# Kernel tuning notes

Hardware: AMD Instinct MI355X
Metric: run time of the kernel (lower is better)

## Reference

```python
import jax, jax.numpy as jnp
import numpy as np

D_MODEL = 1024
BASE = 7
NUM_PLANES = 2
EPS = 1e-6


def setup_inputs() -> dict:
    key = jax.random.key(0)
    k_x, k_w, k_t, k_g = jax.random.split(key, 4)
    B, S, D = 4, 8192, D_MODEL
    x = jax.random.normal(k_x, (B, S, D), dtype=jnp.float32)
    # eidosTransform params: linear 3D -> D, then 2 planes of learned rotation angles over D/2 pairs
    W = jax.random.normal(k_w, (3 * D, D), dtype=jnp.float32) / np.sqrt(3 * D)
    b = jnp.zeros((D,), dtype=jnp.float32)
    theta = jax.random.normal(k_t, (NUM_PLANES, D // 2), dtype=jnp.float32) * 0.1
    # ModularPhaseNorm gain
    gamma = jnp.ones((D,), dtype=jnp.float32)
    return {"x": x, "W": W, "b": b, "theta": theta, "gamma": gamma}


def _eidos_transform(t, W, b, theta):
    # linear projection 3D -> D ('truncate' collapse to d_out)
    y = jnp.einsum("bse,ed->bsd", t, W) + b  # [B,S,D]
    B, S, D = y.shape
    # geometric mode: rotate (even, odd) dim pairs by learned angles, per plane
    for p in range(NUM_PLANES):
        yp = y.reshape(B, S, D // 2, 2)
        a, c2 = yp[..., 0], yp[..., 1]
        cos_t = jnp.cos(theta[p])
        sin_t = jnp.sin(theta[p])
        ra = a * cos_t - c2 * sin_t
        rb = a * sin_t + c2 * cos_t
        y = jnp.stack([ra, rb], axis=-1).reshape(B, S, D)
    return y


def _modular_phase_norm(y, gamma):
    # RMS-normalize within feature groups defined by (dim index mod BASE)
    D = y.shape[-1]
    group = jnp.arange(D) % BASE                      # [D]
    onehot = jax.nn.one_hot(group, BASE, dtype=y.dtype)  # [D, BASE]
    counts = onehot.sum(axis=0)                       # [BASE]
    ss = jnp.einsum("bsd,dg->bsg", y * y, onehot)     # [B,S,BASE]
    rms = jnp.sqrt(ss / counts + EPS)                 # [B,S,BASE]
    denom = rms[..., group]                           # [B,S,D]
    return y / denom * gamma


def reference(x, W, b, theta, gamma):
    B, S, D = x.shape
    zero_row = jnp.zeros((B, 1, D), dtype=x.dtype)
    left = jnp.concatenate([zero_row, x[:, :-1, :]], axis=1)   # roll +1, zero first
    right = jnp.concatenate([x[:, 1:, :], zero_row], axis=1)   # roll -1, zero last
    triplet = jnp.concatenate([left, x, right], axis=-1)        # [B,S,3D]
    mixed = _eidos_transform(triplet, W, b, theta)
    return _modular_phase_norm(mixed, gamma)
```

## Files before the change

kernel.cpp:

```cpp
#include <hip/hip_runtime.h>
#include <hip/hip_bf16.h>
#include <stdint.h>


#define SEQ 8192
#define NB 4
#define DM 1024
#define KD 3072

typedef __attribute__((ext_vector_type(8))) short short8_t;
typedef __attribute__((ext_vector_type(4))) float f32x4;

__device__ __forceinline__ unsigned short f2bf(float f) {
  union { float f; uint32_t u; } v; v.f = f;
  return (unsigned short)((v.u + 0x7fffu + ((v.u >> 16) & 1u)) >> 16);
}

__device__ __forceinline__ void async_ld16(const void* g, void* l) {
  __builtin_amdgcn_global_load_lds(
      (const __attribute__((address_space(1))) uint32_t*)g,
      (__attribute__((address_space(3))) uint32_t*)(uint32_t)(uintptr_t)l,
      16, 0, 0);
}

__global__ __launch_bounds__(256) void prep_w(const float* __restrict__ W,
                                              const float* __restrict__ theta,
                                              unsigned short* __restrict__ Wt) {
  __shared__ float csc[32], css[32];
  __shared__ unsigned short tile[64][72];
  const int bk = blockIdx.x % 48, bn = blockIdx.x / 48;
  const int k0 = bk * 64, n0 = bn * 64;
  const int t = threadIdx.x;
  if (t < 32) {
    int d = n0 / 2 + t;
    float ang = theta[d] + theta[512 + d];
    csc[t] = cosf(ang); css[t] = sinf(ang);
  }
  __syncthreads();
#pragma unroll
  for (int i = 0; i < 8; ++i) {
    int idx = i * 256 + t;
    int pr = idx >> 5;
    int pc = idx & 31;
    const float2 w2 = *(const float2*)&W[(size_t)(k0 + pr) * DM + n0 + pc * 2];
    float c = csc[pc], s = css[pc];
    tile[pc * 2][pr]     = f2bf(w2.x * c - w2.y * s);
    tile[pc * 2 + 1][pr] = f2bf(w2.x * s + w2.y * c);
  }
  __syncthreads();
#pragma unroll
  for (int i = 0; i < 16; ++i) {
    int idx = i * 256 + t;
    int r = idx >> 6, cdx = idx & 63;
    Wt[(size_t)(n0 + r) * KD + k0 + cdx] = tile[r][cdx];
  }
}

__global__ void prep_bias(const float* __restrict__ b, const float* __restrict__ theta,
                          float* __restrict__ biasp, float* __restrict__ zp) {
  const int t = threadIdx.x;
  float ang = theta[t] + theta[512 + t];
  float c = cosf(ang), s = sinf(ang);
  float be = b[2 * t], bo = b[2 * t + 1];
  biasp[2 * t]     = be * c - bo * s;
  biasp[2 * t + 1] = be * s + bo * c;
  if (t < 256) ((float4*)zp)[t] = make_float4(0.f, 0.f, 0.f, 0.f);
}

__global__ __launch_bounds__(256) void prep_x(const float* __restrict__ x,
                                              unsigned short* __restrict__ xbp) {
  const size_t total = (size_t)NB * 8194 * 128;
  for (size_t i = (size_t)blockIdx.x * 256 + threadIdx.x; i < total;
       i += (size_t)gridDim.x * 256) {
    int d8 = (int)(i & 127);
    size_t rem = i >> 7;
    int sp = (int)(rem % 8194);
    size_t bb = rem / 8194;
    uint4 o = make_uint4(0u, 0u, 0u, 0u);
    if (sp > 0 && sp < 8193) {
      const float4* src = (const float4*)(x + (bb * SEQ + (size_t)(sp - 1)) * DM + d8 * 8);
      float4 lo = src[0], hi = src[1];
      o.x = (uint32_t)f2bf(lo.x) | ((uint32_t)f2bf(lo.y) << 16);
      o.y = (uint32_t)f2bf(lo.z) | ((uint32_t)f2bf(lo.w) << 16);
      o.z = (uint32_t)f2bf(hi.x) | ((uint32_t)f2bf(hi.y) << 16);
      o.w = (uint32_t)f2bf(hi.z) | ((uint32_t)f2bf(hi.w) << 16);
    }
    ((uint4*)xbp)[i] = o;
  }
}

__global__ __launch_bounds__(1024, 4) void gemm256(const unsigned short* __restrict__ xbp,
                                                   const unsigned short* __restrict__ Wt,
                                                   const float* __restrict__ biasp,
                                                   float* __restrict__ out) {
  __shared__ __align__(16) unsigned char As[2][16384];
  __shared__ __align__(16) unsigned char Bs[2][16384];

  const int tid = threadIdx.x;
  const int lane = tid & 63;
  const int wid = tid >> 6;
  const int wm = wid >> 2, wn = wid & 3;
  const int row16 = lane & 15, kgrp = lane >> 4;

  const int L = blockIdx.x;
  const int xcd = L & 7;
  const int j = L >> 3;
  const int mtile = xcd * 16 + (j >> 2);
  const int ntile = j & 3;

  const int n0 = ntile * 256;
  const int batch = mtile >> 5;
  const int s0 = (mtile & 31) * 256;
  const size_t m0 = (size_t)mtile * 256;

  int aoff[4], boff[4];
#pragma unroll
  for (int mi = 0; mi < 4; ++mi) {
    int r = wm * 64 + mi * 16 + row16;
    aoff[mi] = r * 64 + (kgrp ^ ((r >> 1) & 3)) * 16;
  }
#pragma unroll
  for (int ni = 0; ni < 4; ++ni) {
    int r = wn * 64 + ni * 16 + row16;
    boff[ni] = r * 64 + (kgrp ^ ((r >> 1) & 3)) * 16;
  }

  const int srow = tid >> 2, sc16 = tid & 3;
  const int scs = sc16 ^ ((srow >> 1) & 3);
  auto stageA = [&](int kt, int buf) {
    const int c = kt >> 5;
    const int ksb = (kt & 31) * 32;
    const size_t base = ((size_t)batch * 8194 + (size_t)(s0 + c)) * DM + ksb;
    async_ld16(xbp + base + (size_t)srow * DM + scs * 8, &As[buf][tid * 16]);
  };
  auto stageB = [&](int kt, int buf) {
    const int kb = kt * 32;
    async_ld16(Wt + (size_t)(n0 + srow) * KD + kb + scs * 8, &Bs[buf][tid * 16]);
  };

  f32x4 acc[4][4];
#pragma unroll
  for (int a = 0; a < 4; ++a)
#pragma unroll
    for (int b = 0; b < 4; ++b) acc[a][b] = (f32x4){0.f, 0.f, 0.f, 0.f};

  stageA(0, 0); stageB(0, 0);
  asm volatile("s_waitcnt vmcnt(0)" ::: "memory");
  __builtin_amdgcn_s_barrier();

  auto body = [&](int kt, int buf, int doStage) {
    if (doStage) { stageA(kt + 1, buf ^ 1); stageB(kt + 1, buf ^ 1); }
    short8_t af[4], bf[4];
#pragma unroll
    for (int mi = 0; mi < 4; ++mi)
      af[mi] = *(const short8_t*)(&As[buf][0] + aoff[mi]);
#pragma unroll
    for (int ni = 0; ni < 4; ++ni)
      bf[ni] = *(const short8_t*)(&Bs[buf][0] + boff[ni]);
    asm volatile("s_waitcnt lgkmcnt(0)" ::: "memory");
    __builtin_amdgcn_sched_barrier(0);
    __builtin_amdgcn_s_setprio(1);
#pragma unroll
    for (int mi = 0; mi < 4; ++mi)
#pragma unroll
      for (int ni = 0; ni < 4; ++ni)
        acc[mi][ni] = __builtin_amdgcn_mfma_f32_16x16x32_bf16(
            af[mi], bf[ni], acc[mi][ni], 0, 0, 0);
    __builtin_amdgcn_s_setprio(0);
    asm volatile("s_waitcnt vmcnt(0)" ::: "memory");
    __builtin_amdgcn_sched_barrier(0);
    __builtin_amdgcn_s_barrier();
  };

  for (int kt2 = 0; kt2 < 94; kt2 += 2) {
    body(kt2 + 0, 0, 1);
    body(kt2 + 1, 1, 1);
  }
  body(94, 0, 1);
  body(95, 1, 0);

#pragma unroll
  for (int mi = 0; mi < 4; ++mi) {
    size_t grow = m0 + (size_t)(wm * 64 + mi * 16 + kgrp * 4);
#pragma unroll
    for (int ni = 0; ni < 4; ++ni) {
      int col = n0 + wn * 64 + ni * 16 + row16;
      float bia = biasp[col];
      float* op = out + grow * DM + col;
#pragma unroll
      for (int r = 0; r < 4; ++r) op[(size_t)r * DM] = acc[mi][ni][r] + bia;
    }
  }
}

__global__ __launch_bounds__(256) void gemm_fb(const float* __restrict__ Ag,
                                               const unsigned short* __restrict__ Wt,
                                               const float* __restrict__ biasp,
                                               const float* __restrict__ zp,
                                               float* __restrict__ out) {
  __shared__ __align__(16) unsigned char As[128 * 64 * 4];
  __shared__ __align__(16) unsigned char Bs[128 * 64 * 2];

  const int tid = threadIdx.x;
  const int lane = tid & 63;
  const int wid = tid >> 6;
  const int wm = wid >> 1, wn = wid & 1;
  const int row16 = lane & 15, kgrp = lane >> 4;

  const int L = blockIdx.x;
  const int xcd = L & 7;
  const int j = L >> 3;
  const int mtile = xcd * 32 + (j >> 3);
  const int ntile = j & 7;

  const int n0 = ntile * 128;
  const int batch = mtile >> 6;
  const int s0 = (mtile & 63) * 128;
  const size_t m0 = (size_t)mtile * 128;

  f32x4 acc[4][4];
#pragma unroll
  for (int a = 0; a < 4; ++a)
#pragma unroll
    for (int b = 0; b < 4; ++b) acc[a][b] = (f32x4){0.f, 0.f, 0.f, 0.f};

  for (int kt = 0; kt < 48; ++kt) {
    const int c = kt >> 4;
    const int ksb = (kt & 15) * 64;
    __syncthreads();
#pragma unroll
    for (int it = 0; it < 8; ++it) {
      int f16 = it * 256 + tid;
      int row = f16 >> 4, c16 = f16 & 15;
      int c16s = c16 ^ (row & 7);
      int s = s0 + row + c - 1;
      const float* src = (s >= 0 && s < SEQ)
          ? Ag + ((size_t)batch * SEQ + (size_t)s) * DM + ksb + c16s * 4
          : zp + c16s * 4;
      async_ld16(src, As + f16 * 16);
    }
#pragma unroll
    for (int it = 0; it < 4; ++it) {
      int f16 = it * 256 + tid;
      int row = f16 >> 3, c16 = f16 & 7;
      int c16s = c16 ^ (row & 7);
      const unsigned short* src = Wt + (size_t)(n0 + row) * KD + kt * 64 + c16s * 8;
      async_ld16(src, Bs + f16 * 16);
    }
    __syncthreads();

#pragma unroll
    for (int kk = 0; kk < 2; ++kk) {
      short8_t af[4], bfr[4];
#pragma unroll
      for (int mi = 0; mi < 4; ++mi) {
        int r = wm * 64 + mi * 16 + row16;
        int kb = kk * 128 + kgrp * 32;
        f32x4 lo = *(const f32x4*)(As + r * 256 + (kb ^ ((r & 7) << 4)));
        f32x4 hi = *(const f32x4*)(As + r * 256 + ((kb + 16) ^ ((r & 7) << 4)));
        union { short8_t v; unsigned short u[8]; } pk;
        pk.u[0] = f2bf(lo[0]); pk.u[1] = f2bf(lo[1]);
        pk.u[2] = f2bf(lo[2]); pk.u[3] = f2bf(lo[3]);
        pk.u[4] = f2bf(hi[0]); pk.u[5] = f2bf(hi[1]);
        pk.u[6] = f2bf(hi[2]); pk.u[7] = f2bf(hi[3]);
        af[mi] = pk.v;
      }
#pragma unroll
      for (int ni = 0; ni < 4; ++ni) {
        int r = wn * 64 + ni * 16 + row16;
        int kb = kk * 64 + kgrp * 16;
        bfr[ni] = *(const short8_t*)(Bs + r * 128 + (kb ^ ((r & 7) << 4)));
      }
#pragma unroll
      for (int mi = 0; mi < 4; ++mi)
#pragma unroll
        for (int ni = 0; ni < 4; ++ni)
          acc[mi][ni] = __builtin_amdgcn_mfma_f32_16x16x32_bf16(
              af[mi], bfr[ni], acc[mi][ni], 0, 0, 0);
    }
  }

#pragma unroll
  for (int mi = 0; mi < 4; ++mi) {
    size_t grow = m0 + (size_t)(wm * 64 + mi * 16 + kgrp * 4);
#pragma unroll
    for (int ni = 0; ni < 4; ++ni) {
      int col = n0 + wn * 64 + ni * 16 + row16;
      float bia = biasp[col];
      float* op = out + grow * DM + col;
#pragma unroll
      for (int r = 0; r < 4; ++r) op[(size_t)r * DM] = acc[mi][ni][r] + bia;
    }
  }
}

__global__ __launch_bounds__(256) void norm_kernel(float* __restrict__ y,
                                                   const float* __restrict__ gamma) {
  const int tid = threadIdx.x, lane = tid & 63, wv = tid >> 6;
  const size_t row = (size_t)blockIdx.x * 4 + wv;
  float4* rp = (float4*)(y + row * DM);
  const float4* gp = (const float4*)gamma;
  float4 v[4];
#pragma unroll
  for (int jj = 0; jj < 4; ++jj) v[jj] = rp[jj * 64 + lane];

  float ss[7] = {0.f, 0.f, 0.f, 0.f, 0.f, 0.f, 0.f};
#pragma unroll
  for (int jj = 0; jj < 4; ++jj) {
    const float vv[4] = {v[jj].x, v[jj].y, v[jj].z, v[jj].w};
#pragma unroll
    for (int i = 0; i < 4; ++i) {
      int d = (jj * 64 + lane) * 4 + i;
      int g = d % 7;
      float sq = vv[i] * vv[i];
#pragma unroll
      for (int t = 0; t < 7; ++t) ss[t] += (g == t) ? sq : 0.f;
    }
  }
#pragma unroll
  for (int t = 0; t < 7; ++t) {
#pragma unroll
    for (int off = 32; off >= 1; off >>= 1) ss[t] += __shfl_xor(ss[t], off, 64);
  }
  float inv[7];
#pragma unroll
  for (int t = 0; t < 7; ++t) {
    float cnt = (t < 2) ? 147.f : 146.f;
    inv[t] = rsqrtf(ss[t] / cnt + 1e-6f);
  }
#pragma unroll
  for (int jj = 0; jj < 4; ++jj) {
    float4 g4 = gp[jj * 64 + lane];
    const float vv[4] = {v[jj].x, v[jj].y, v[jj].z, v[jj].w};
    const float gg[4] = {g4.x, g4.y, g4.z, g4.w};
    float o[4];
#pragma unroll
    for (int i = 0; i < 4; ++i) {
      int d = (jj * 64 + lane) * 4 + i;
      int g = d % 7;
      float iv = inv[0];
#pragma unroll
      for (int t = 1; t < 7; ++t) iv = (g == t) ? inv[t] : iv;
      o[i] = vv[i] * iv * gg[i];
    }
    rp[jj * 64 + lane] = make_float4(o[0], o[1], o[2], o[3]);
  }
}

extern "C" void kernel_launch(void* const* d_in, const int* in_sizes, int n_in,
                              void* d_out, int out_size, void* d_ws, size_t ws_size,
                              hipStream_t stream) {
  const float* x     = (const float*)d_in[0];
  const float* W     = (const float*)d_in[1];
  const float* b     = (const float*)d_in[2];
  const float* theta = (const float*)d_in[3];
  const float* gamma = (const float*)d_in[4];
  float* out = (float*)d_out;
  (void)in_sizes; (void)n_in; (void)out_size;

  char* ws = (char*)d_ws;
  unsigned short* Wt = (unsigned short*)ws;
  float* biasp = (float*)(ws + 6291456);
  float* zp    = (float*)(ws + 6291456 + 4096);
  unsigned short* xbp = (unsigned short*)(ws + 6299648);
  const size_t needA = 6299648 + (size_t)NB * 8194 * DM * 2;

  prep_w<<<dim3(768), dim3(256), 0, stream>>>(W, theta, Wt);
  prep_bias<<<dim3(1), dim3(512), 0, stream>>>(b, theta, biasp, zp);

  if (ws_size >= needA) {
    prep_x<<<dim3(4096), dim3(256), 0, stream>>>(x, xbp);
    gemm256<<<dim3(512), dim3(1024), 0, stream>>>(xbp, Wt, biasp, out);
  } else {
    gemm_fb<<<dim3(2048), dim3(256), 0, stream>>>(x, Wt, biasp, zp, out);
  }
  norm_kernel<<<dim3(8192), dim3(256), 0, stream>>>(out, gamma);
}
```

Baseline: 265.8 us.

## Use 256x128 GEMM tiles with 512 threads and triple-buffered prefetch

Shrinks the GEMM block tile from 256x256 with 1024 threads to 256x128 with 512 threads, doubling the grid to 1024 blocks. LDS staging moves from double to triple buffering with a prefetch distance of two k-steps, and the waits become partial vmcnt waits so global loads overlap more of the MFMA work. In exchange, the smaller N tile lowers arithmetic intensity and re-reads each A tile across twice as many blocks. The larger LDS footprint per block may also limit how many blocks fit on a CU.

```diff
diff --git a/kernel.cpp b/kernel.cpp
--- a/kernel.cpp
+++ b/kernel.cpp
@@ -89,26 +89,26 @@
   }
 }
 
-__global__ __launch_bounds__(1024, 4) void gemm256(const unsigned short* __restrict__ xbp,
-                                                   const unsigned short* __restrict__ Wt,
-                                                   const float* __restrict__ biasp,
-                                                   float* __restrict__ out) {
-  __shared__ __align__(16) unsigned char As[2][16384];
-  __shared__ __align__(16) unsigned char Bs[2][16384];
+__global__ __launch_bounds__(512, 4) void gemm256(const unsigned short* __restrict__ xbp,
+                                                  const unsigned short* __restrict__ Wt,
+                                                  const float* __restrict__ biasp,
+                                                  float* __restrict__ out) {
+  __shared__ __align__(16) unsigned char As[3][16384];
+  __shared__ __align__(16) unsigned char Bs[3][8192];
 
   const int tid = threadIdx.x;
   const int lane = tid & 63;
   const int wid = tid >> 6;
-  const int wm = wid >> 2, wn = wid & 3;
+  const int wm = wid >> 1, wn = wid & 1;
   const int row16 = lane & 15, kgrp = lane >> 4;
 
   const int L = blockIdx.x;
   const int xcd = L & 7;
   const int j = L >> 3;
-  const int mtile = xcd * 16 + (j >> 2);
-  const int ntile = j & 3;
-
-  const int n0 = ntile * 256;
+  const int mtile = xcd * 16 + (j >> 3);
+  const int ntile = j & 7;
+
+  const int n0 = ntile * 128;
   const int batch = mtile >> 5;
   const int s0 = (mtile & 31) * 256;
   const size_t m0 = (size_t)mtile * 256;
@@ -125,17 +125,23 @@
     boff[ni] = r * 64 + (kgrp ^ ((r >> 1) & 3)) * 16;
   }
 
-  const int srow = tid >> 2, sc16 = tid & 3;
-  const int scs = sc16 ^ ((srow >> 1) & 3);
   auto stageA = [&](int kt, int buf) {
     const int c = kt >> 5;
     const int ksb = (kt & 31) * 32;
     const size_t base = ((size_t)batch * 8194 + (size_t)(s0 + c)) * DM + ksb;
-    async_ld16(xbp + base + (size_t)srow * DM + scs * 8, &As[buf][tid * 16]);
+#pragma unroll
+    for (int i = 0; i < 2; ++i) {
+      int idx = i * 512 + tid;
+      int row = idx >> 2, c16 = idx & 3;
+      int cs = c16 ^ ((row >> 1) & 3);
+      async_ld16(xbp + base + (size_t)row * DM + cs * 8, &As[buf][idx * 16]);
+    }
   };
   auto stageB = [&](int kt, int buf) {
     const int kb = kt * 32;
-    async_ld16(Wt + (size_t)(n0 + srow) * KD + kb + scs * 8, &Bs[buf][tid * 16]);
+    int row = tid >> 2, c16 = tid & 3;
+    int cs = c16 ^ ((row >> 1) & 3);
+    async_ld16(Wt + (size_t)(n0 + row) * KD + kb + cs * 8, &Bs[buf][tid * 16]);
   };
 
   f32x4 acc[4][4];
@@ -145,11 +151,16 @@
     for (int b = 0; b < 4; ++b) acc[a][b] = (f32x4){0.f, 0.f, 0.f, 0.f};
 
   stageA(0, 0); stageB(0, 0);
-  asm volatile("s_waitcnt vmcnt(0)" ::: "memory");
+  stageA(1, 1); stageB(1, 1);
+  stageA(2, 2); stageB(2, 2);
+  asm volatile("s_waitcnt vmcnt(6)" ::: "memory");
   __builtin_amdgcn_s_barrier();
 
-  auto body = [&](int kt, int buf, int doStage) {
-    if (doStage) { stageA(kt + 1, buf ^ 1); stageB(kt + 1, buf ^ 1); }
+  auto body = [&](int kt, int buf, int doStage, int vmN) {
+    if (doStage) {
+      const int sbuf = (buf + 2) % 3;
+      stageA(kt + 2, sbuf); stageB(kt + 2, sbuf);
+    }
     short8_t af[4], bf[4];
 #pragma unroll
     for (int mi = 0; mi < 4; ++mi)
@@ -167,17 +178,20 @@
         acc[mi][ni] = __builtin_amdgcn_mfma_f32_16x16x32_bf16(
             af[mi], bf[ni], acc[mi][ni], 0, 0, 0);
     __builtin_amdgcn_s_setprio(0);
-    asm volatile("s_waitcnt vmcnt(0)" ::: "memory");
+    if (vmN == 3)      asm volatile("s_waitcnt vmcnt(3)" ::: "memory");
+    else               asm volatile("s_waitcnt vmcnt(0)" ::: "memory");
     __builtin_amdgcn_sched_barrier(0);
     __builtin_amdgcn_s_barrier();
   };
 
-  for (int kt2 = 0; kt2 < 94; kt2 += 2) {
-    body(kt2 + 0, 0, 1);
-    body(kt2 + 1, 1, 1);
-  }
-  body(94, 0, 1);
-  body(95, 1, 0);
+  for (int kt3 = 0; kt3 < 93; kt3 += 3) {
+    body(kt3 + 0, 0, 1, 3);
+    body(kt3 + 1, 1, 1, 3);
+    body(kt3 + 2, 2, 1, 3);
+  }
+  body(93, 0, 1, 3);
+  body(94, 1, 0, 0);
+  body(95, 2, 0, 0);
 
 #pragma unroll
   for (int mi = 0; mi < 4; ++mi) {
@@ -370,7 +384,7 @@
 
   if (ws_size >= needA) {
     prep_x<<<dim3(4096), dim3(256), 0, stream>>>(x, xbp);
-    gemm256<<<dim3(512), dim3(1024), 0, stream>>>(xbp, Wt, biasp, out);
+    gemm256<<<dim3(1024), dim3(512), 0, stream>>>(xbp, Wt, biasp, out);
   } else {
     gemm_fb<<<dim3(2048), dim3(256), 0, stream>>>(x, Wt, biasp, zp, out);
   }
```

Measured after the change: 281.5 us. +5.9%, slower.

## Restructure GEMM to 8 waves with larger per-wave tiles and ping-pong pipeline

Applied to the files above, without the earlier changes.

Moves the 256x256 GEMM block from 16 waves to 8, so each wave computes a 128x64 output tile with twice the accumulators. The K step grows to 64 and the LDS layout is split into half-tiles with an XOR swizzle over 8 chunks. Global-to-LDS staging is interleaved into an 8-phase schedule that overlaps loads with MFMA work across two buffers. The goal is more MFMA per LDS read and fewer barriers per unit of work, at the cost of higher register pressure and lower occupancy.

```diff
diff --git a/kernel.cpp b/kernel.cpp
--- a/kernel.cpp
+++ b/kernel.cpp
@@ -89,12 +89,12 @@
   }
 }
 
-__global__ __launch_bounds__(1024, 4) void gemm256(const unsigned short* __restrict__ xbp,
-                                                   const unsigned short* __restrict__ Wt,
-                                                   const float* __restrict__ biasp,
-                                                   float* __restrict__ out) {
-  __shared__ __align__(16) unsigned char As[2][16384];
-  __shared__ __align__(16) unsigned char Bs[2][16384];
+__global__ __launch_bounds__(512, 2) void gemm256(const unsigned short* __restrict__ xbp,
+                                                  const unsigned short* __restrict__ Wt,
+                                                  const float* __restrict__ biasp,
+                                                  float* __restrict__ out) {
+  __shared__ __align__(16) unsigned char As[2][2][16384];
+  __shared__ __align__(16) unsigned char Bs[2][2][16384];
 
   const int tid = threadIdx.x;
   const int lane = tid & 63;
@@ -113,75 +113,103 @@
   const int s0 = (mtile & 31) * 256;
   const size_t m0 = (size_t)mtile * 256;
 
-  int aoff[4], boff[4];
-#pragma unroll
-  for (int mi = 0; mi < 4; ++mi) {
-    int r = wm * 64 + mi * 16 + row16;
-    aoff[mi] = r * 64 + (kgrp ^ ((r >> 1) & 3)) * 16;
-  }
-#pragma unroll
-  for (int ni = 0; ni < 4; ++ni) {
-    int r = wn * 64 + ni * 16 + row16;
-    boff[ni] = r * 64 + (kgrp ^ ((r >> 1) & 3)) * 16;
-  }
-
-  const int srow = tid >> 2, sc16 = tid & 3;
-  const int scs = sc16 ^ ((srow >> 1) & 3);
-  auto stageA = [&](int kt, int buf) {
-    const int c = kt >> 5;
-    const int ksb = (kt & 31) * 32;
-    const size_t base = ((size_t)batch * 8194 + (size_t)(s0 + c)) * DM + ksb;
-    async_ld16(xbp + base + (size_t)srow * DM + scs * 8, &As[buf][tid * 16]);
+  auto stageA = [&](int kt, int db) {
+    const int c = kt >> 4, ksb = (kt & 15) * 64;
+    const size_t base =
+        ((size_t)batch * 8194 + (size_t)(s0 + wm * 128 + c)) * DM + ksb;
+    unsigned char* dst = &As[db][wm][0] + wn * 4096;
+#pragma unroll
+    for (int i = 0; i < 4; ++i) {
+      int idx = wn * 256 + i * 64 + lane;
+      int row = idx >> 3, ch = idx & 7;
+      int cs = ch ^ (row & 7);
+      async_ld16(xbp + base + (size_t)row * DM + cs * 8,
+                 dst + (i * 64 + lane) * 16);
+    }
   };
-  auto stageB = [&](int kt, int buf) {
-    const int kb = kt * 32;
-    async_ld16(Wt + (size_t)(n0 + srow) * KD + kb + scs * 8, &Bs[buf][tid * 16]);
+  auto stageB = [&](int kt, int db) {
+    const int hb = wn >> 1, sl = wm * 2 + (wn & 1);
+    unsigned char* dst = &Bs[db][hb][0] + sl * 4096;
+#pragma unroll
+    for (int i = 0; i < 4; ++i) {
+      int idx = sl * 256 + i * 64 + lane;
+      int row = idx >> 3, ch = idx & 7;
+      int cs = ch ^ (row & 7);
+      async_ld16(Wt + (size_t)(n0 + hb * 128 + row) * KD + kt * 64 + cs * 8,
+                 dst + (i * 64 + lane) * 16);
+    }
   };
 
-  f32x4 acc[4][4];
-#pragma unroll
-  for (int a = 0; a < 4; ++a)
+  f32x4 acc[8][4];
+#pragma unroll
+  for (int a = 0; a < 8; ++a)
 #pragma unroll
     for (int b = 0; b < 4; ++b) acc[a][b] = (f32x4){0.f, 0.f, 0.f, 0.f};
 
+  short8_t a4[4], b4[4];
+
+  auto rdA = [&](int db, int q, int s) {
+    const unsigned char* base = &As[db][wm][0];
+#pragma unroll
+    for (int mi = 0; mi < 4; ++mi) {
+      int r = (q * 4 + mi) * 16 + row16;
+      a4[mi] = *(const short8_t*)(base + r * 128 +
+                                  (((s << 2) | kgrp) ^ (r & 7)) * 16);
+    }
+  };
+  auto rdB = [&](int db, int s) {
+    const unsigned char* base = &Bs[db][wn >> 1][0];
+#pragma unroll
+    for (int ni = 0; ni < 4; ++ni) {
+      int r = (wn & 1) * 64 + ni * 16 + row16;
+      b4[ni] = *(const short8_t*)(base + r * 128 +
+                                  (((s << 2) | kgrp) ^ (r & 7)) * 16);
+    }
+  };
+  auto mma = [&](int q) {
+    __builtin_amdgcn_s_setprio(1);
+#pragma unroll
+    for (int mi = 0; mi < 4; ++mi)
+#pragma unroll
+      for (int ni = 0; ni < 4; ++ni)
+        acc[q * 4 + mi][ni] = __builtin_amdgcn_mfma_f32_16x16x32_bf16(
+            a4[mi], b4[ni], acc[q * 4 + mi][ni], 0, 0, 0);
+    __builtin_amdgcn_s_setprio(0);
+  };
+
   stageA(0, 0); stageB(0, 0);
-  asm volatile("s_waitcnt vmcnt(0)" ::: "memory");
+  stageA(1, 1); stageB(1, 1);
+  asm volatile("s_waitcnt vmcnt(8)" ::: "memory");
   __builtin_amdgcn_s_barrier();
 
-  auto body = [&](int kt, int buf, int doStage) {
-    if (doStage) { stageA(kt + 1, buf ^ 1); stageB(kt + 1, buf ^ 1); }
-    short8_t af[4], bf[4];
-#pragma unroll
-    for (int mi = 0; mi < 4; ++mi)
-      af[mi] = *(const short8_t*)(&As[buf][0] + aoff[mi]);
-#pragma unroll
-    for (int ni = 0; ni < 4; ++ni)
-      bf[ni] = *(const short8_t*)(&Bs[buf][0] + boff[ni]);
-    asm volatile("s_waitcnt lgkmcnt(0)" ::: "memory");
-    __builtin_amdgcn_sched_barrier(0);
-    __builtin_amdgcn_s_setprio(1);
-#pragma unroll
-    for (int mi = 0; mi < 4; ++mi)
-#pragma unroll
-      for (int ni = 0; ni < 4; ++ni)
-        acc[mi][ni] = __builtin_amdgcn_mfma_f32_16x16x32_bf16(
-            af[mi], bf[ni], acc[mi][ni], 0, 0, 0);
-    __builtin_amdgcn_s_setprio(0);
-    asm volatile("s_waitcnt vmcnt(0)" ::: "memory");
-    __builtin_amdgcn_sched_barrier(0);
-    __builtin_amdgcn_s_barrier();
-  };
-
-  for (int kt2 = 0; kt2 < 94; kt2 += 2) {
-    body(kt2 + 0, 0, 1);
-    body(kt2 + 1, 1, 1);
-  }
-  body(94, 0, 1);
-  body(95, 1, 0);
-
-#pragma unroll
-  for (int mi = 0; mi < 4; ++mi) {
-    size_t grow = m0 + (size_t)(wm * 64 + mi * 16 + kgrp * 4);
+  for (int it = 0; it < 24; ++it) {
+    const int k0s = 2 * it;
+    const int k1s = 2 * it + 1;
+#pragma unroll
+    for (int ph = 0; ph < 8; ++ph) {
+      const int db = ph >> 2;
+      const int q  = ph & 1;
+      const int s  = (ph >> 1) & 1;
+      if (ph == 0) { if (it > 0) stageA(k1s, 1); }
+      else if (ph == 2) { if (it > 0) stageB(k1s, 1); }
+      else if (ph == 4) { if (it < 23) stageA(k0s + 2, 0); }
+      else if (ph == 6) { if (it < 23) stageB(k0s + 2, 0); }
+      rdA(db, q, s);
+      if (q == 0) rdB(db, s);
+      __builtin_amdgcn_s_barrier();
+      asm volatile("s_waitcnt lgkmcnt(0)" ::: "memory");
+      __builtin_amdgcn_sched_barrier(0);
+      mma(q);
+      if (ph == 3 || ph == 7)
+        asm volatile("s_waitcnt vmcnt(0)" ::: "memory");
+      __builtin_amdgcn_sched_barrier(0);
+      __builtin_amdgcn_s_barrier();
+    }
+  }
+
+#pragma unroll
+  for (int mi = 0; mi < 8; ++mi) {
+    size_t grow = m0 + (size_t)(wm * 128 + mi * 16 + kgrp * 4);
 #pragma unroll
     for (int ni = 0; ni < 4; ++ni) {
       int col = n0 + wn * 64 + ni * 16 + row16;
@@ -370,7 +398,7 @@
 
   if (ws_size >= needA) {
     prep_x<<<dim3(4096), dim3(256), 0, stream>>>(x, xbp);
-    gemm256<<<dim3(512), dim3(1024), 0, stream>>>(xbp, Wt, biasp, out);
+    gemm256<<<dim3(512), dim3(512), 0, stream>>>(xbp, Wt, biasp, out);
   } else {
     gemm_fb<<<dim3(2048), dim3(256), 0, stream>>>(x, Wt, biasp, zp, out);
   }
```

Result: faster. 259.6 us (-2.4%).
